# Optimization experiments

Hardware: AMD Instinct MI355X
Metric: run time of the kernel (lower is better)

Reference implementation:

```python
import jax, jax.numpy as jnp
import numpy as np

B, T, V, E, H = 64, 512, 32000, 256, 256


def _gru_scan(xp, h0, rkernel, rbias):
    # xp: [T,B,3H] precomputed input projections (incl. input bias)
    # Keras GRUCell with reset_after=True semantics.
    def step(h, xpt):
        hp = h @ rkernel + rbias            # [B,3H]
        xz, xr, xh = jnp.split(xpt, 3, axis=-1)
        hz, hr, hh = jnp.split(hp, 3, axis=-1)
        z = jax.nn.sigmoid(xz + hz)
        r = jax.nn.sigmoid(xr + hr)
        hc = jnp.tanh(xh + r * hh)
        hn = z * h + (1.0 - z) * hc
        return hn, hn
    return jax.lax.scan(step, h0, xp)


def setup_inputs() -> dict:
    key = jax.random.key(0)
    ks = jax.random.split(key, 8)
    s_in = 1.0 / np.sqrt(E)
    s_rec = 1.0 / np.sqrt(H)
    return {
        "x": jax.random.randint(ks[0], (B, T), 0, V, dtype=jnp.int32),
        "hidden": jnp.zeros((B, H), jnp.float32),
        "emb": jax.random.normal(ks[1], (V, E), jnp.float32) * 0.05,
        "kernel_f": jax.random.normal(ks[2], (E, 3 * H), jnp.float32) * s_in,
        "rkernel_f": jax.random.normal(ks[3], (H, 3 * H), jnp.float32) * s_rec,
        "bias_f": jnp.zeros((2, 3 * H), jnp.float32),
        "kernel_b": jax.random.normal(ks[4], (E, 3 * H), jnp.float32) * s_in,
        "rkernel_b": jax.random.normal(ks[5], (H, 3 * H), jnp.float32) * s_rec,
        "bias_b": jnp.zeros((2, 3 * H), jnp.float32),
    }


def reference(x, hidden, emb, kernel_f, rkernel_f, bias_f, kernel_b, rkernel_b, bias_b):
    e = emb[x]                                   # [B,T,E] embedding lookup

    def run(kernel, rkernel, bias, reverse):
        xp = jnp.einsum('bte,eh->tbh', e, kernel) + bias[0]  # [T,B,3H]
        if reverse:
            xp = xp[::-1]
        hT, ys = _gru_scan(xp, hidden, rkernel, bias[1])
        ys = jnp.swapaxes(ys, 0, 1)              # [B,T,H]
        if reverse:
            ys = ys[:, ::-1]
        return hT, ys

    h_f, y_f = run(kernel_f, rkernel_f, bias_f, False)
    h_b, y_b = run(kernel_b, rkernel_b, bias_b, True)
    concatenated = jnp.concatenate([y_f, y_b], axis=-1)  # [B,T,2H]
    return concatenated, h_f, h_b
```

## Files before the change

kernel.cpp:

```cpp
#include <hip/hip_runtime.h>
#include <hip/hip_bf16.h>

typedef _Float16 h2v __attribute__((ext_vector_type(2)));

#define B_SZ 64
#define T_SZ 512
#define E_SZ 256
#define H_SZ 256
#define C_SZ 768

__device__ __forceinline__ float dot2f(h2v a, h2v b, float c) {
#if __has_builtin(__builtin_amdgcn_fdot2)
  return __builtin_amdgcn_fdot2(a, b, c, false);
#else
  return c + (float)a[0] * (float)b[0] + (float)a[1] * (float)b[1];
#endif
}

__device__ __forceinline__ float rcp_fast(float x) {
  return __builtin_amdgcn_rcpf(x);
}

__device__ __forceinline__ float dpp_add_x1(float v) {
  int i = __builtin_bit_cast(int, v);
  int s = __builtin_amdgcn_update_dpp(i, i, 0xB1, 0xF, 0xF, true);
  return v + __builtin_bit_cast(float, s);
}
__device__ __forceinline__ float dpp_add_x2(float v) {
  int i = __builtin_bit_cast(int, v);
  int s = __builtin_amdgcn_update_dpp(i, i, 0x4E, 0xF, 0xF, true);
  return v + __builtin_bit_cast(float, s);
}

__global__ __launch_bounds__(256) void xp_gemm_kernel(
    const int* __restrict__ x,
    const float* __restrict__ emb,
    const float* __restrict__ kf, const float* __restrict__ bf,
    const float* __restrict__ kb, const float* __restrict__ bb,
    _Float16* __restrict__ xp)
{
  const int ct  = blockIdx.x;
  const int rt  = blockIdx.y;
  const int dir = blockIdx.z;
  const float* Kp = dir ? kb : kf;
  const float* Bp = dir ? bb : bf;
  const int c0 = ct * 48;
  const int r0 = rt * 64;
  const int tid = threadIdx.x;

  __shared__ __align__(16) _Float16 As[64][264];
  __shared__ __align__(16) _Float16 Bs[48][264];

  for (int r = 0; r < 64; ++r) {
    int xi = x[r0 + r];
    As[r][tid] = (_Float16)emb[(size_t)xi * E_SZ + tid];
  }
  for (int i = tid; i < 48 * 256; i += 256) {
    int k = i / 48;
    int c = i - k * 48;
    Bs[c][k] = (_Float16)Kp[k * C_SZ + c0 + c];
  }
  __syncthreads();

  const int tr = tid >> 4;
  const int tc = tid & 15;
  float acc[4][3];
  #pragma unroll
  for (int i = 0; i < 4; ++i)
    #pragma unroll
    for (int j = 0; j < 3; ++j) acc[i][j] = 0.f;

  #pragma unroll
  for (int m = 0; m < 32; ++m) {
    float4 a4[4], b4[3];
    #pragma unroll
    for (int i = 0; i < 4; ++i) a4[i] = *(const float4*)&As[tr * 4 + i][m * 8];
    #pragma unroll
    for (int j = 0; j < 3; ++j) b4[j] = *(const float4*)&Bs[tc + 16 * j][m * 8];
    #pragma unroll
    for (int i = 0; i < 4; ++i) {
      const h2v* ah = (const h2v*)&a4[i];
      #pragma unroll
      for (int j = 0; j < 3; ++j) {
        const h2v* bh = (const h2v*)&b4[j];
        #pragma unroll
        for (int p = 0; p < 4; ++p) acc[i][j] = dot2f(ah[p], bh[p], acc[i][j]);
      }
    }
  }

  #pragma unroll
  for (int j = 0; j < 3; ++j) {
    int c = c0 + tc + 16 * j;
    float bias = Bp[c];
    #pragma unroll
    for (int i = 0; i < 4; ++i) {
      int r = r0 + tr * 4 + i;
      xp[((size_t)dir * (B_SZ * T_SZ) + r) * C_SZ + c] = (_Float16)(acc[i][j] + bias);
    }
  }
}

__global__ __launch_bounds__(768) __attribute__((amdgpu_waves_per_eu(3, 3)))
void gru_scan_kernel(
    const float* __restrict__ hidden,
    const float* __restrict__ rkf, const float* __restrict__ bf,
    const float* __restrict__ rkb, const float* __restrict__ bb,
    const _Float16* __restrict__ xp,
    float* __restrict__ out)
{
  const int b   = blockIdx.x;
  const int dir = blockIdx.y;
  const int tid = threadIdx.x;
  const int q   = tid & 3;
  const float* RK = dir ? rkb : rkf;
  const float* BS = dir ? bb : bf;

  __shared__ __align__(16) _Float16 hbuf[4 * 72];
  __shared__ __align__(16) float hp[C_SZ];

  h2v col[4][32];
  const int cbase = tid & ~3;
  #pragma unroll
  for (int o = 0; o < 4; ++o) {
    #pragma unroll
    for (int m = 0; m < 32; ++m) {
      int k = 64 * q + 2 * m;
      volatile const float* rk0 = RK + (size_t)k * C_SZ + cbase + o;
      volatile const float* rk1 = RK + (size_t)(k + 1) * C_SZ + cbase + o;
      h2v c2;
      c2[0] = (_Float16)(*rk0);
      c2[1] = (_Float16)(*rk1);
      col[o][m] = c2;
    }
  }
  #pragma unroll
  for (int o = 0; o < 4; ++o)
    #pragma unroll
    for (int m = 0; m < 32; ++m)
      asm volatile("" : "+v"(col[o][m]));

  const float rb = BS[C_SZ + tid];

  float hreg = 0.f;
  if (tid < H_SZ) {
    hreg = hidden[b * H_SZ + tid];
    hbuf[72 * (tid >> 6) + (tid & 63)] = (_Float16)hreg;
  }

  const size_t xbase = ((size_t)dir * (B_SZ * T_SZ) + (size_t)b * T_SZ) * C_SZ;
  float xz_c = 0.f, xr_c = 0.f, xh_c = 0.f;
  if (tid < H_SZ) {
    int t0 = dir ? (T_SZ - 1) : 0;
    const _Float16* xr0 = xp + xbase + (size_t)t0 * C_SZ;
    xz_c = (float)xr0[tid];
    xr_c = (float)xr0[tid + H_SZ];
    xh_c = (float)xr0[tid + 2 * H_SZ];
  }
  __syncthreads();

  for (int s = 0; s < T_SZ; ++s) {
    float xz_n = 0.f, xr_n = 0.f, xh_n = 0.f;
    if (tid < H_SZ) {
      int sn = (s + 1 < T_SZ) ? (s + 1) : s;
      int tn = dir ? (T_SZ - 1 - sn) : sn;
      const _Float16* xrn = xp + xbase + (size_t)tn * C_SZ;
      xz_n = (float)xrn[tid];
      xr_n = (float)xrn[tid + H_SZ];
      xh_n = (float)xrn[tid + 2 * H_SZ];
    }

    float acc0 = 0.f, acc1 = 0.f, acc2 = 0.f, acc3 = 0.f;
    const float4* hsl = (const float4*)(hbuf + 72 * q);
    #pragma unroll
    for (int i = 0; i < 8; ++i) {
      float4 c = hsl[i];
      const h2v* hv = (const h2v*)&c;
      #pragma unroll
      for (int p = 0; p < 4; ++p) {
        int m = 4 * i + p;
        acc0 = dot2f(hv[p], col[0][m], acc0);
        acc1 = dot2f(hv[p], col[1][m], acc1);
        acc2 = dot2f(hv[p], col[2][m], acc2);
        acc3 = dot2f(hv[p], col[3][m], acc3);
      }
    }
    acc0 = dpp_add_x2(dpp_add_x1(acc0));
    acc1 = dpp_add_x2(dpp_add_x1(acc1));
    acc2 = dpp_add_x2(dpp_add_x1(acc2));
    acc3 = dpp_add_x2(dpp_add_x1(acc3));
    float sel01 = (q & 1) ? acc1 : acc0;
    float sel23 = (q & 1) ? acc3 : acc2;
    float val   = (q & 2) ? sel23 : sel01;
    hp[tid] = val + rb;
    __syncthreads();

    if (tid < H_SZ) {
      float z  = rcp_fast(1.f + __expf(-(xz_c + hp[tid])));
      float r  = rcp_fast(1.f + __expf(-(xr_c + hp[tid + H_SZ])));
      float pre = xh_c + r * hp[tid + 2 * H_SZ];
      float e2 = __expf(2.f * pre);
      float hc = 1.f - 2.f * rcp_fast(e2 + 1.f);
      hreg = z * hreg + (1.f - z) * hc;
      int t = dir ? (T_SZ - 1 - s) : s;
      out[((size_t)b * T_SZ + t) * (2 * H_SZ) + dir * H_SZ + tid] = hreg;
      hbuf[72 * (tid >> 6) + (tid & 63)] = (_Float16)hreg;
    }
    __syncthreads();

    xz_c = xz_n; xr_c = xr_n; xh_c = xh_n;
  }

  if (tid < H_SZ) {
    out[(size_t)(B_SZ * T_SZ) * (2 * H_SZ) + dir * (B_SZ * H_SZ) + b * H_SZ + tid] = hreg;
  }
}

extern "C" void kernel_launch(void* const* d_in, const int* in_sizes, int n_in,
                              void* d_out, int out_size, void* d_ws, size_t ws_size,
                              hipStream_t stream) {
  const int*   x    = (const int*)d_in[0];
  const float* hid  = (const float*)d_in[1];
  const float* emb  = (const float*)d_in[2];
  const float* kf   = (const float*)d_in[3];
  const float* rkf  = (const float*)d_in[4];
  const float* bf   = (const float*)d_in[5];
  const float* kb   = (const float*)d_in[6];
  const float* rkb  = (const float*)d_in[7];
  const float* bb   = (const float*)d_in[8];
  float* out = (float*)d_out;

  _Float16* xp = (_Float16*)d_ws;

  dim3 g1(16, 512, 2);
  xp_gemm_kernel<<<g1, 256, 0, stream>>>(x, emb, kf, bf, kb, bb, xp);

  dim3 g2(B_SZ, 2);
  gru_scan_kernel<<<g2, 768, 0, stream>>>(hid, rkf, bf, rkb, bb, xp, out);
}
```

Baseline: 1.090 ms.

## Repartition GRU recurrent matvec to 512 threads with two-way K split

Measured after the change: 1.175 ms. 1.08x slower.

```diff
diff --git a/kernel.cpp b/kernel.cpp
--- a/kernel.cpp
+++ b/kernel.cpp
@@ -24,11 +24,6 @@
 __device__ __forceinline__ float dpp_add_x1(float v) {
   int i = __builtin_bit_cast(int, v);
   int s = __builtin_amdgcn_update_dpp(i, i, 0xB1, 0xF, 0xF, true);
-  return v + __builtin_bit_cast(float, s);
-}
-__device__ __forceinline__ float dpp_add_x2(float v) {
-  int i = __builtin_bit_cast(int, v);
-  int s = __builtin_amdgcn_update_dpp(i, i, 0x4E, 0xF, 0xF, true);
   return v + __builtin_bit_cast(float, s);
 }
 
@@ -101,7 +96,7 @@
   }
 }
 
-__global__ __launch_bounds__(768) __attribute__((amdgpu_waves_per_eu(3, 3)))
+__global__ __launch_bounds__(512) __attribute__((amdgpu_waves_per_eu(2, 2)))
 void gru_scan_kernel(
     const float* __restrict__ hidden,
     const float* __restrict__ rkf, const float* __restrict__ bf,
@@ -109,23 +104,24 @@
     const _Float16* __restrict__ xp,
     float* __restrict__ out)
 {
-  const int b   = blockIdx.x;
-  const int dir = blockIdx.y;
-  const int tid = threadIdx.x;
-  const int q   = tid & 3;
+  const int b    = blockIdx.x;
+  const int dir  = blockIdx.y;
+  const int tid  = threadIdx.x;
+  const int pair = tid >> 1;
+  const int half = tid & 1;
   const float* RK = dir ? rkb : rkf;
   const float* BS = dir ? bb : bf;
 
-  __shared__ __align__(16) _Float16 hbuf[4 * 72];
+  __shared__ __align__(16) _Float16 hbuf[2 * 136];
   __shared__ __align__(16) float hp[C_SZ];
 
-  h2v col[4][32];
-  const int cbase = tid & ~3;
-  #pragma unroll
-  for (int o = 0; o < 4; ++o) {
-    #pragma unroll
-    for (int m = 0; m < 32; ++m) {
-      int k = 64 * q + 2 * m;
+  h2v col[3][64];
+  const int cbase = 3 * pair;
+  #pragma unroll
+  for (int o = 0; o < 3; ++o) {
+    #pragma unroll
+    for (int m = 0; m < 64; ++m) {
+      int k = 128 * half + 2 * m;
       volatile const float* rk0 = RK + (size_t)k * C_SZ + cbase + o;
       volatile const float* rk1 = RK + (size_t)(k + 1) * C_SZ + cbase + o;
       h2v c2;
@@ -135,17 +131,19 @@
     }
   }
   #pragma unroll
-  for (int o = 0; o < 4; ++o)
-    #pragma unroll
-    for (int m = 0; m < 32; ++m)
+  for (int o = 0; o < 3; ++o)
+    #pragma unroll
+    for (int m = 0; m < 64; ++m)
       asm volatile("" : "+v"(col[o][m]));
 
-  const float rb = BS[C_SZ + tid];
+  float rb0 = BS[C_SZ + cbase + 0];
+  float rb1 = BS[C_SZ + cbase + 1];
+  float rb2 = BS[C_SZ + cbase + 2];
 
   float hreg = 0.f;
   if (tid < H_SZ) {
     hreg = hidden[b * H_SZ + tid];
-    hbuf[72 * (tid >> 6) + (tid & 63)] = (_Float16)hreg;
+    hbuf[136 * (tid >> 7) + (tid & 127)] = (_Float16)hreg;
   }
 
   const size_t xbase = ((size_t)dir * (B_SZ * T_SZ) + (size_t)b * T_SZ) * C_SZ;
@@ -170,29 +168,44 @@
       xh_n = (float)xrn[tid + 2 * H_SZ];
     }
 
-    float acc0 = 0.f, acc1 = 0.f, acc2 = 0.f, acc3 = 0.f;
-    const float4* hsl = (const float4*)(hbuf + 72 * q);
-    #pragma unroll
-    for (int i = 0; i < 8; ++i) {
-      float4 c = hsl[i];
-      const h2v* hv = (const h2v*)&c;
+    float acc0 = 0.f, acc1 = 0.f, acc2 = 0.f;
+    const float4* hsl = (const float4*)(hbuf + 136 * half);
+    #pragma unroll
+    for (int c4 = 0; c4 < 4; ++c4) {
+      float4 q0 = hsl[4 * c4 + 0];
+      float4 q1 = hsl[4 * c4 + 1];
+      float4 q2 = hsl[4 * c4 + 2];
+      float4 q3 = hsl[4 * c4 + 3];
+      const h2v* h0 = (const h2v*)&q0;
+      const h2v* h1 = (const h2v*)&q1;
+      const h2v* h2 = (const h2v*)&q2;
+      const h2v* h3 = (const h2v*)&q3;
+      int mb = 16 * c4;
       #pragma unroll
       for (int p = 0; p < 4; ++p) {
-        int m = 4 * i + p;
-        acc0 = dot2f(hv[p], col[0][m], acc0);
-        acc1 = dot2f(hv[p], col[1][m], acc1);
-        acc2 = dot2f(hv[p], col[2][m], acc2);
-        acc3 = dot2f(hv[p], col[3][m], acc3);
+        acc0 = dot2f(h0[p], col[0][mb + p], acc0);
+        acc1 = dot2f(h0[p], col[1][mb + p], acc1);
+        acc2 = dot2f(h0[p], col[2][mb + p], acc2);
+        acc0 = dot2f(h1[p], col[0][mb + 4 + p], acc0);
+        acc1 = dot2f(h1[p], col[1][mb + 4 + p], acc1);
+        acc2 = dot2f(h1[p], col[2][mb + 4 + p], acc2);
+        acc0 = dot2f(h2[p], col[0][mb + 8 + p], acc0);
+        acc1 = dot2f(h2[p], col[1][mb + 8 + p], acc1);
+        acc2 = dot2f(h2[p], col[2][mb + 8 + p], acc2);
+        acc0 = dot2f(h3[p], col[0][mb + 12 + p], acc0);
+        acc1 = dot2f(h3[p], col[1][mb + 12 + p], acc1);
+        acc2 = dot2f(h3[p], col[2][mb + 12 + p], acc2);
       }
     }
-    acc0 = dpp_add_x2(dpp_add_x1(acc0));
-    acc1 = dpp_add_x2(dpp_add_x1(acc1));
-    acc2 = dpp_add_x2(dpp_add_x1(acc2));
-    acc3 = dpp_add_x2(dpp_add_x1(acc3));
-    float sel01 = (q & 1) ? acc1 : acc0;
-    float sel23 = (q & 1) ? acc3 : acc2;
-    float val   = (q & 2) ? sel23 : sel01;
-    hp[tid] = val + rb;
+    acc0 = dpp_add_x1(acc0);
+    acc1 = dpp_add_x1(acc1);
+    acc2 = dpp_add_x1(acc2);
+    if (half == 0) {
+      hp[cbase + 0] = acc0 + rb0;
+      hp[cbase + 1] = acc1 + rb1;
+    } else {
+      hp[cbase + 2] = acc2 + rb2;
+    }
     __syncthreads();
 
     if (tid < H_SZ) {
@@ -204,7 +217,7 @@
       hreg = z * hreg + (1.f - z) * hc;
       int t = dir ? (T_SZ - 1 - s) : s;
       out[((size_t)b * T_SZ + t) * (2 * H_SZ) + dir * H_SZ + tid] = hreg;
-      hbuf[72 * (tid >> 6) + (tid & 63)] = (_Float16)hreg;
+      hbuf[136 * (tid >> 7) + (tid & 127)] = (_Float16)hreg;
     }
     __syncthreads();
 
@@ -236,5 +249,5 @@
   xp_gemm_kernel<<<g1, 256, 0, stream>>>(x, emb, kf, bf, kb, bb, xp);
 
   dim3 g2(B_SZ, 2);
-  gru_scan_kernel<<<g2, 768, 0, stream>>>(hid, rkf, bf, rkb, bb, xp, out);
-}
+  gru_scan_kernel<<<g2, 512, 0, stream>>>(hid, rkf, bf, rkb, bb, xp, out);
+}
```
